# Performance work log

Hardware: AMD Instinct MI355X
Metric: run time of the kernel (lower is better)

Reference implementation:

```python
import jax, jax.numpy as jnp
import numpy as np

B, N, FIN, FOUT, H = 8, 2048, 128, 128, 2


def setup_inputs() -> dict:
    key = jax.random.key(0)
    k_h, k_adj, k_w, k_a = jax.random.split(key, 4)
    h = jax.random.normal(k_h, (B, N, FIN), dtype=jnp.float32)
    adj = jax.random.randint(k_adj, (B, N, N), 0, 2).astype(jnp.int32)
    # self-loops so no softmax row is all -inf
    idx = jnp.arange(N)
    adj = adj.at[:, idx, idx].set(1)
    W = jax.random.normal(k_w, (H, FIN, FOUT), dtype=jnp.float32) * 0.1
    a = jax.random.normal(k_a, (H, 2 * FOUT), dtype=jnp.float32) * 0.1
    return {"h": h, "adj": adj, "W": W, "a": a}


def reference(h, adj, W, a):
    # h: [B,N,FIN], adj: [B,N,N] int, W: [H,FIN,FOUT], a: [H,2*FOUT]
    Fout = W.shape[-1]
    Wh = jnp.einsum('bnf,hfo->bhno', h, W)              # [B,H,N,FOUT]
    # decompose a^T [Wh_i || Wh_j] = a1.Wh_i + a2.Wh_j (exact same math,
    # avoids the [B,N,N,2F] concat the torch code materializes)
    a1, a2 = a[:, :Fout], a[:, Fout:]
    s_i = jnp.einsum('bhno,ho->bhn', Wh, a1)            # score from node i
    s_j = jnp.einsum('bhno,ho->bhn', Wh, a2)            # score from node j
    e = jax.nn.leaky_relu(s_i[:, :, :, None] + s_j[:, :, None, :], 0.2)  # [B,H,N,N]
    e = jnp.where(adj[:, None, :, :] == 0, -jnp.inf, e)
    att = jax.nn.softmax(e, axis=-1)                    # [B,H,N,N]
    out = jnp.einsum('bhnm,bhmo->bhno', att, Wh)        # [B,H,N,FOUT]
    b, hh, n, f = out.shape
    # concat heads along feature dim (head order matches torch cat)
    return out.transpose(0, 2, 1, 3).reshape(b, n, hh * f)
```

## Files before the change

### kernel.cpp

```cpp
#include <hip/hip_runtime.h>
#include <math.h>

constexpr int Bv   = 8;
constexpr int Nv   = 2048;
constexpr int FIN  = 128;
constexpr int FOUT = 128;
constexpr int NH   = 2;
constexpr float LOG2E = 1.44269504088896340736f;

typedef __attribute__((ext_vector_type(8)))  short short8;
typedef __attribute__((ext_vector_type(4)))  float f32x4;
typedef __attribute__((ext_vector_type(16))) float f32x16;
typedef __attribute__((ext_vector_type(4)))  int   i32x4;
typedef unsigned long long u64;

typedef __attribute__((address_space(1))) const void GCV;
typedef __attribute__((address_space(3))) void LV;

static __device__ __forceinline__ unsigned short f2bf(float f) {
    unsigned u = __builtin_bit_cast(unsigned, f);
    u += 0x7fffu + ((u >> 16) & 1u);
    return (unsigned short)(u >> 16);
}
static __device__ __forceinline__ float bf2f(unsigned short s) {
    unsigned u = ((unsigned)s) << 16;
    return __builtin_bit_cast(float, u);
}
static __device__ __forceinline__ float fast_exp2(float x) {
#if __has_builtin(__builtin_amdgcn_exp2f)
    return __builtin_amdgcn_exp2f(x);
#else
    return exp2f(x);
#endif
}
static __device__ __forceinline__ unsigned cvt_pk_bf16(float lo, float hi) {
    unsigned r;
    asm("v_cvt_pk_bf16_f32 %0, %1, %2" : "=v"(r) : "v"(lo), "v"(hi));
    return r;
}

__global__ __launch_bounds__(256) void wa_kernel(const float* __restrict__ W,
                                                 const float* __restrict__ a,
                                                 float* __restrict__ wa,
                                                 unsigned short* __restrict__ wthi,
                                                 unsigned short* __restrict__ wtlo) {
    __shared__ unsigned short shi[FIN * 132];
    __shared__ unsigned short slo[FIN * 132];
    int hh = blockIdx.x;
    int t = threadIdx.x;

    const float* Ws = W + (size_t)hh * FIN * FOUT;
    for (int idx = t; idx < FIN * FOUT; idx += 256) {
        int f = idx >> 7, o = idx & 127;
        float wv = Ws[idx];
        unsigned short uh = f2bf(wv);
        shi[o * 132 + f] = uh;
        slo[o * 132 + f] = f2bf(wv - bf2f(uh));
    }

    int f = t >> 1, half = t & 1;
    const float* Wr = Ws + (size_t)f * FOUT + half * 64;
    const float* ar = a + (size_t)hh * 2 * FOUT + half * 64;
    float s1 = 0.f, s2 = 0.f;
    for (int o = 0; o < 64; o += 4) {
        float4 w4 = *(const float4*)&Wr[o];
        s1 += w4.x * ar[o] + w4.y * ar[o + 1] + w4.z * ar[o + 2] + w4.w * ar[o + 3];
        s2 += w4.x * ar[FOUT + o] + w4.y * ar[FOUT + o + 1] + w4.z * ar[FOUT + o + 2] + w4.w * ar[FOUT + o + 3];
    }
    s1 += __shfl_xor(s1, 1, 64);
    s2 += __shfl_xor(s2, 1, 64);
    if (half == 0) {
        wa[(hh * 2 + 0) * FIN + f] = s1 * LOG2E;
        wa[(hh * 2 + 1) * FIN + f] = s2 * LOG2E;
    }

    __syncthreads();
    unsigned short* dhi = wthi + (size_t)hh * FOUT * FIN;
    unsigned short* dlo = wtlo + (size_t)hh * FOUT * FIN;
    for (int idx = t; idx < FIN * FOUT; idx += 256) {
        int o = idx >> 7, ff = idx & 127;
        dhi[idx] = shi[o * 132 + ff];
        dlo[idx] = slo[o * 132 + ff];
    }
}

__global__ __launch_bounds__(256, 4) void prep2_kernel(
    const float* __restrict__ h, const float* __restrict__ wa,
    const unsigned short* __restrict__ wthi, const unsigned short* __restrict__ wtlo,
    unsigned short* __restrict__ whf, float* __restrict__ si, float* __restrict__ sj) {
    int bid = blockIdx.x;
    int t   = threadIdx.x;

    if (bid < 4096) {
        int row  = bid * 4 + (t >> 6);
        int lane = t & 63;
        float x0 = h[(size_t)row * FIN + lane];
        float x1 = h[(size_t)row * FIN + 64 + lane];
        float s[4];
#pragma unroll
        for (int q = 0; q < 4; ++q) {
            const float* wp = wa + q * FIN;
            s[q] = x0 * wp[lane] + x1 * wp[64 + lane];
        }
#pragma unroll
        for (int m = 32; m >= 1; m >>= 1) {
#pragma unroll
            for (int q = 0; q < 4; ++q) s[q] += __shfl_xor(s[q], m, 64);
        }
        if (lane == 0) {
            int bb = row >> 11, n = row & (Nv - 1);
            si[((size_t)(bb * NH + 0)) * Nv + n] = s[0];
            sj[((size_t)(bb * NH + 0)) * Nv + n] = s[1];
            si[((size_t)(bb * NH + 1)) * Nv + n] = s[2];
            sj[((size_t)(bb * NH + 1)) * Nv + n] = s[3];
        }
    } else {
        int wb2 = bid - 4096;
        int bb  = wb2 & 7;
        int r2  = wb2 >> 3;
        int hh  = r2 & 1;
        int jtb = r2 >> 1;
        int n0  = jtb * 64;

        int w = t >> 6, l = t & 63, lo16 = l & 15, grp = l >> 4;
        int o0 = w * 32;

        const unsigned short* Whi = wthi + (size_t)hh * FOUT * FIN;
        const unsigned short* Wlo = wtlo + (size_t)hh * FOUT * FIN;
        short8 ahi[2][4], alo[2][4];
#pragma unroll
        for (int ot = 0; ot < 2; ++ot)
#pragma unroll
            for (int kt = 0; kt < 4; ++kt) {
                int off = (o0 + ot * 16 + lo16) * FIN + kt * 32 + grp * 8;
                ahi[ot][kt] = *(const short8*)&Whi[off];
                alo[ot][kt] = *(const short8*)&Wlo[off];
            }

        f32x4 acc[2][4];
#pragma unroll
        for (int ot = 0; ot < 2; ++ot)
#pragma unroll
            for (int nt = 0; nt < 4; ++nt) acc[ot][nt] = (f32x4){0.f, 0.f, 0.f, 0.f};

        const float* hb = h + ((size_t)bb * Nv + n0) * FIN;
#pragma unroll
        for (int nt = 0; nt < 4; ++nt) {
#pragma unroll
            for (int kt = 0; kt < 4; ++kt) {
                const float* hp = hb + (size_t)(nt * 16 + lo16) * FIN + kt * 32 + grp * 8;
                float4 x0 = *(const float4*)hp;
                float4 x1 = *(const float4*)(hp + 4);
                float xs[8] = {x0.x, x0.y, x0.z, x0.w, x1.x, x1.y, x1.z, x1.w};
                short8 bhi, blo;
#pragma unroll
                for (int i = 0; i < 8; ++i) {
                    unsigned short uh = f2bf(xs[i]);
                    bhi[i] = (short)uh;
                    blo[i] = (short)f2bf(xs[i] - bf2f(uh));
                }
#pragma unroll
                for (int ot = 0; ot < 2; ++ot) {
                    acc[ot][nt] = __builtin_amdgcn_mfma_f32_16x16x32_bf16(ahi[ot][kt], bhi, acc[ot][nt], 0, 0, 0);
                    acc[ot][nt] = __builtin_amdgcn_mfma_f32_16x16x32_bf16(ahi[ot][kt], blo, acc[ot][nt], 0, 0, 0);
                    acc[ot][nt] = __builtin_amdgcn_mfma_f32_16x16x32_bf16(alo[ot][kt], bhi, acc[ot][nt], 0, 0, 0);
                }
            }
        }
        unsigned short* db = whf + (size_t)(bb * NH + hh) * 262144;
#pragma unroll
        for (int ot = 0; ot < 2; ++ot)
#pragma unroll
            for (int nt = 0; nt < 4; ++nt)
#pragma unroll
                for (int reg = 0; reg < 4; ++reg) {
                    int oc = ot * 16 + grp * 4 + reg;
                    db[(size_t)(((jtb * 4 + nt) * 4 + w) * 64 + (lo16 >> 3) * 32 + oc) * 8 + (lo16 & 7)] =
                        f2bf(acc[ot][nt][reg]);
                }
    }
}

__global__ __launch_bounds__(256, 2) void gat_mega_kernel(
    const int* __restrict__ adj, const unsigned short* __restrict__ whf,
    const float* __restrict__ si, const float* __restrict__ sj,
    float* __restrict__ out) {
    __shared__ int abuf[2][2][2048];
    __shared__ u64 mlds[32][33];

    int bid = blockIdx.x;
    int bb  = bid & 7;
    int rp  = bid >> 3;
    int r0  = rp * 32;

    int t = threadIdx.x, w = t >> 6, l = t & 63;

    {
        int wr = w >> 1;
        int wsg = w & 1;
        const int* base = adj + ((size_t)bb * Nv + r0) * Nv;

        auto issue = [&](int buf, int c) {
            const int* src = base + (size_t)(c * 2 + wr) * Nv + wsg * 1024 + l * 4;
            LV* dst = (LV*)&abuf[buf][wr][wsg * 1024];
#pragma unroll
            for (int k = 0; k < 4; ++k) {
                __builtin_amdgcn_global_load_lds((GCV*)(src + k * 256),
                                                 (LV*)((char*)dst + k * 1024), 16, 0, 0);
            }
        };

        issue(0, 0);
        int buf = 0;
        for (int c = 0; c < 16; ++c) {
            if (c < 15) issue(buf ^ 1, c + 1);
            if (c < 15) { asm volatile("s_waitcnt vmcnt(4)" ::: "memory"); }
            else        { asm volatile("s_waitcnt vmcnt(0)" ::: "memory"); }
            __builtin_amdgcn_sched_barrier(0);
            u64 myval = 0;
#pragma unroll
            for (int j16 = 0; j16 < 16; ++j16) {
                int jt = wsg * 16 + j16;
                int iv = abuf[buf][wr][jt * 64 + l];
                u64 bal = __ballot(iv != 0);
                if (l == j16) myval = bal;
            }
            if (l < 16) mlds[c * 2 + wr][wsg * 16 + l] = myval;
            buf ^= 1;
        }
    }
    __syncthreads();

    int hh = w >> 1, ch = w & 1;
    int lo32 = l & 31, kh = l >> 5;
    int myrow = r0 + lo32;

    float sir = si[(size_t)(bb * NH + hh) * Nv + myrow];
    const float* sjb  = sj + (size_t)(bb * NH + hh) * Nv;
    const unsigned short* wbp = whf + (size_t)(bb * NH + hh) * 262144 + (size_t)l * 8;

    f32x16 acc0, acc1, accL;
#pragma unroll
    for (int i = 0; i < 16; ++i) { acc0[i] = 0.f; acc1[i] = 0.f; accL[i] = 0.f; }

    const int ones_w = 0x3f803f80;
    short8 onesf = __builtin_bit_cast(short8, (i32x4){ones_w, ones_w, ones_w, ones_w});

    for (int jt = 0; jt < 32; ++jt) {
        int jb = jt * 64;
        const unsigned short* fb = wbp + (size_t)(jt * 16 + ch * 2) * 512;
        short8 bf[4][2];
#pragma unroll
        for (int kt = 0; kt < 4; ++kt) {
            bf[kt][0] = *(const short8*)(fb + (kt * 4 + 0) * 512);
            bf[kt][1] = *(const short8*)(fb + (kt * 4 + 1) * 512);
        }
        u64 mcur = mlds[lo32][jt];

        short8 af[4];
#pragma unroll
        for (int kt = 0; kt < 4; ++kt) {
            unsigned mb = (unsigned)(mcur >> (kt * 16 + kh * 8)) & 0xFFu;
            const float* sp = &sjb[jb + kt * 16 + kh * 8];
            float4 s0 = *(const float4*)sp;
            float4 s1 = *(const float4*)(sp + 4);
            float x0 = sir + s0.x, x1 = sir + s0.y, x2 = sir + s0.z, x3 = sir + s0.w;
            float x4 = sir + s1.x, x5 = sir + s1.y, x6 = sir + s1.z, x7 = sir + s1.w;
            x0 = fmaxf(x0, 0.2f * x0); x1 = fmaxf(x1, 0.2f * x1);
            x2 = fmaxf(x2, 0.2f * x2); x3 = fmaxf(x3, 0.2f * x3);
            x4 = fmaxf(x4, 0.2f * x4); x5 = fmaxf(x5, 0.2f * x5);
            x6 = fmaxf(x6, 0.2f * x6); x7 = fmaxf(x7, 0.2f * x7);
            float p0 = fast_exp2(x0), p1 = fast_exp2(x1), p2 = fast_exp2(x2), p3 = fast_exp2(x3);
            float p4 = fast_exp2(x4), p5 = fast_exp2(x5), p6 = fast_exp2(x6), p7 = fast_exp2(x7);
            p0 = (mb & 1u)   ? p0 : 0.f;  p1 = (mb & 2u)   ? p1 : 0.f;
            p2 = (mb & 4u)   ? p2 : 0.f;  p3 = (mb & 8u)   ? p3 : 0.f;
            p4 = (mb & 16u)  ? p4 : 0.f;  p5 = (mb & 32u)  ? p5 : 0.f;
            p6 = (mb & 64u)  ? p6 : 0.f;  p7 = (mb & 128u) ? p7 : 0.f;
            unsigned w0 = cvt_pk_bf16(p0, p1), w1 = cvt_pk_bf16(p2, p3);
            unsigned w2 = cvt_pk_bf16(p4, p5), w3 = cvt_pk_bf16(p6, p7);
            af[kt] = __builtin_bit_cast(short8, (i32x4){(int)w0, (int)w1, (int)w2, (int)w3});
        }
#pragma unroll
        for (int kt = 0; kt < 4; ++kt) {
            acc0 = __builtin_amdgcn_mfma_f32_32x32x16_bf16(af[kt], bf[kt][0], acc0, 0, 0, 0);
            acc1 = __builtin_amdgcn_mfma_f32_32x32x16_bf16(af[kt], bf[kt][1], acc1, 0, 0, 0);
            accL = __builtin_amdgcn_mfma_f32_32x32x16_bf16(af[kt], onesf,    accL, 0, 0, 0);
        }
    }

#pragma unroll
    for (int reg = 0; reg < 16; ++reg) {
        int rowc = (reg & 3) + 8 * (reg >> 2) + 4 * kh;
        float linv = 1.0f / accL[reg];
        float* op = out + ((size_t)(bb * Nv + r0 + rowc)) * (NH * FOUT) + hh * FOUT + ch * 64;
        op[lo32]      = acc0[reg] * linv;
        op[32 + lo32] = acc1[reg] * linv;
    }
}

extern "C" void kernel_launch(void* const* d_in, const int* in_sizes, int n_in,
                              void* d_out, int out_size, void* d_ws, size_t ws_size,
                              hipStream_t stream) {
    const float* h   = (const float*)d_in[0];
    const int*   adj = (const int*)d_in[1];
    const float* W   = (const float*)d_in[2];
    const float* a   = (const float*)d_in[3];
    float*       out = (float*)d_out;

    char* ws = (char*)d_ws;
    unsigned short* whf  = (unsigned short*)ws;
    float* si = (float*)(ws + 8388608);
    float* sj = si + (size_t)Bv * NH * Nv;
    float* wa = sj + (size_t)Bv * NH * Nv;
    unsigned short* wthi = (unsigned short*)(wa + NH * 2 * FIN);
    unsigned short* wtlo = wthi + (size_t)NH * FOUT * FIN;

    wa_kernel   <<<dim3(2),    dim3(256), 0, stream>>>(W, a, wa, wthi, wtlo);
    prep2_kernel<<<dim3(4608), dim3(256), 0, stream>>>(h, wa, wthi, wtlo, whf, si, sj);
    gat_mega_kernel<<<dim3(512), dim3(256), 0, stream>>>(adj, whf, si, sj, out);
}
```

Before: 107.5 us.

## Interleave adjacency mask streaming with attention MFMA loop

The kernel no longer packs the whole 32x2048 adjacency tile into bitmasks before starting compute. Each iteration now loads a 32x128 column chunk through a double-buffered global_load_lds pipeline, ballots it into a per-buffer mask, synchronizes, and runs the softmax-weighted MFMAs for those two 64-column tiles. The goal is to hide the large adjacency read behind the exp/MFMA work and to cut LDS use, which may allow more occupancy. The cost is a __syncthreads every chunk, and it relies on the vmcnt accounting still covering the outstanding loads correctly.

```diff
diff --git a/kernel.cpp b/kernel.cpp
--- a/kernel.cpp
+++ b/kernel.cpp
@@ -185,8 +185,8 @@
     const int* __restrict__ adj, const unsigned short* __restrict__ whf,
     const float* __restrict__ si, const float* __restrict__ sj,
     float* __restrict__ out) {
-    __shared__ int abuf[2][2][2048];
-    __shared__ u64 mlds[32][33];
+    __shared__ int abuf[2][32][128];
+    __shared__ u64 mlds[2][32][2];
 
     int bid = blockIdx.x;
     int bb  = bid & 7;
@@ -194,47 +194,21 @@
     int r0  = rp * 32;
 
     int t = threadIdx.x, w = t >> 6, l = t & 63;
-
-    {
-        int wr = w >> 1;
-        int wsg = w & 1;
-        const int* base = adj + ((size_t)bb * Nv + r0) * Nv;
-
-        auto issue = [&](int buf, int c) {
-            const int* src = base + (size_t)(c * 2 + wr) * Nv + wsg * 1024 + l * 4;
-            LV* dst = (LV*)&abuf[buf][wr][wsg * 1024];
-#pragma unroll
-            for (int k = 0; k < 4; ++k) {
-                __builtin_amdgcn_global_load_lds((GCV*)(src + k * 256),
-                                                 (LV*)((char*)dst + k * 1024), 16, 0, 0);
-            }
-        };
-
-        issue(0, 0);
-        int buf = 0;
-        for (int c = 0; c < 16; ++c) {
-            if (c < 15) issue(buf ^ 1, c + 1);
-            if (c < 15) { asm volatile("s_waitcnt vmcnt(4)" ::: "memory"); }
-            else        { asm volatile("s_waitcnt vmcnt(0)" ::: "memory"); }
-            __builtin_amdgcn_sched_barrier(0);
-            u64 myval = 0;
-#pragma unroll
-            for (int j16 = 0; j16 < 16; ++j16) {
-                int jt = wsg * 16 + j16;
-                int iv = abuf[buf][wr][jt * 64 + l];
-                u64 bal = __ballot(iv != 0);
-                if (l == j16) myval = bal;
-            }
-            if (l < 16) mlds[c * 2 + wr][wsg * 16 + l] = myval;
-            buf ^= 1;
-        }
-    }
-    __syncthreads();
-
     int hh = w >> 1, ch = w & 1;
     int lo32 = l & 31, kh = l >> 5;
     int myrow = r0 + lo32;
 
+    const int* gbase = adj + ((size_t)bb * Nv + r0 + w * 8) * Nv;
+
+    auto issue = [&](int buf, int c) {
+#pragma unroll
+        for (int k = 0; k < 4; ++k) {
+            const int* src = gbase + (size_t)(2 * k + (l >> 5)) * Nv + c * 128 + (l & 31) * 4;
+            LV* dst = (LV*)&abuf[buf][w * 8 + 2 * k][0];
+            __builtin_amdgcn_global_load_lds((GCV*)src, dst, 16, 0, 0);
+        }
+    };
+
     float sir = si[(size_t)(bb * NH + hh) * Nv + myrow];
     const float* sjb  = sj + (size_t)(bb * NH + hh) * Nv;
     const unsigned short* wbp = whf + (size_t)(bb * NH + hh) * 262144 + (size_t)l * 8;
@@ -246,46 +220,71 @@
     const int ones_w = 0x3f803f80;
     short8 onesf = __builtin_bit_cast(short8, (i32x4){ones_w, ones_w, ones_w, ones_w});
 
-    for (int jt = 0; jt < 32; ++jt) {
-        int jb = jt * 64;
-        const unsigned short* fb = wbp + (size_t)(jt * 16 + ch * 2) * 512;
-        short8 bf[4][2];
-#pragma unroll
-        for (int kt = 0; kt < 4; ++kt) {
-            bf[kt][0] = *(const short8*)(fb + (kt * 4 + 0) * 512);
-            bf[kt][1] = *(const short8*)(fb + (kt * 4 + 1) * 512);
-        }
-        u64 mcur = mlds[lo32][jt];
-
-        short8 af[4];
-#pragma unroll
-        for (int kt = 0; kt < 4; ++kt) {
-            unsigned mb = (unsigned)(mcur >> (kt * 16 + kh * 8)) & 0xFFu;
-            const float* sp = &sjb[jb + kt * 16 + kh * 8];
-            float4 s0 = *(const float4*)sp;
-            float4 s1 = *(const float4*)(sp + 4);
-            float x0 = sir + s0.x, x1 = sir + s0.y, x2 = sir + s0.z, x3 = sir + s0.w;
-            float x4 = sir + s1.x, x5 = sir + s1.y, x6 = sir + s1.z, x7 = sir + s1.w;
-            x0 = fmaxf(x0, 0.2f * x0); x1 = fmaxf(x1, 0.2f * x1);
-            x2 = fmaxf(x2, 0.2f * x2); x3 = fmaxf(x3, 0.2f * x3);
-            x4 = fmaxf(x4, 0.2f * x4); x5 = fmaxf(x5, 0.2f * x5);
-            x6 = fmaxf(x6, 0.2f * x6); x7 = fmaxf(x7, 0.2f * x7);
-            float p0 = fast_exp2(x0), p1 = fast_exp2(x1), p2 = fast_exp2(x2), p3 = fast_exp2(x3);
-            float p4 = fast_exp2(x4), p5 = fast_exp2(x5), p6 = fast_exp2(x6), p7 = fast_exp2(x7);
-            p0 = (mb & 1u)   ? p0 : 0.f;  p1 = (mb & 2u)   ? p1 : 0.f;
-            p2 = (mb & 4u)   ? p2 : 0.f;  p3 = (mb & 8u)   ? p3 : 0.f;
-            p4 = (mb & 16u)  ? p4 : 0.f;  p5 = (mb & 32u)  ? p5 : 0.f;
-            p6 = (mb & 64u)  ? p6 : 0.f;  p7 = (mb & 128u) ? p7 : 0.f;
-            unsigned w0 = cvt_pk_bf16(p0, p1), w1 = cvt_pk_bf16(p2, p3);
-            unsigned w2 = cvt_pk_bf16(p4, p5), w3 = cvt_pk_bf16(p6, p7);
-            af[kt] = __builtin_bit_cast(short8, (i32x4){(int)w0, (int)w1, (int)w2, (int)w3});
-        }
-#pragma unroll
-        for (int kt = 0; kt < 4; ++kt) {
-            acc0 = __builtin_amdgcn_mfma_f32_32x32x16_bf16(af[kt], bf[kt][0], acc0, 0, 0, 0);
-            acc1 = __builtin_amdgcn_mfma_f32_32x32x16_bf16(af[kt], bf[kt][1], acc1, 0, 0, 0);
-            accL = __builtin_amdgcn_mfma_f32_32x32x16_bf16(af[kt], onesf,    accL, 0, 0, 0);
-        }
+    issue(0, 0);
+    int buf = 0;
+    for (int c = 0; c < 16; ++c) {
+        if (c < 15) {
+            issue(buf ^ 1, c + 1);
+            asm volatile("s_waitcnt vmcnt(4)" ::: "memory");
+        } else {
+            asm volatile("s_waitcnt vmcnt(0)" ::: "memory");
+        }
+        __builtin_amdgcn_sched_barrier(0);
+#pragma unroll
+        for (int r = 0; r < 8; ++r) {
+            int row = w * 8 + r;
+#pragma unroll
+            for (int q = 0; q < 2; ++q) {
+                int iv = abuf[buf][row][q * 64 + l];
+                u64 bal = __ballot(iv != 0);
+                if (l == 0) mlds[buf][row][q] = bal;
+            }
+        }
+        __syncthreads();
+#pragma unroll
+        for (int q = 0; q < 2; ++q) {
+            int jt = 2 * c + q;
+            int jb = jt * 64;
+            const unsigned short* fb = wbp + (size_t)(jt * 16 + ch * 2) * 512;
+            short8 bf[4][2];
+#pragma unroll
+            for (int kt = 0; kt < 4; ++kt) {
+                bf[kt][0] = *(const short8*)(fb + (kt * 4 + 0) * 512);
+                bf[kt][1] = *(const short8*)(fb + (kt * 4 + 1) * 512);
+            }
+            u64 mcur = mlds[buf][lo32][q];
+
+            short8 af[4];
+#pragma unroll
+            for (int kt = 0; kt < 4; ++kt) {
+                unsigned mb = (unsigned)(mcur >> (kt * 16 + kh * 8)) & 0xFFu;
+                const float* sp = &sjb[jb + kt * 16 + kh * 8];
+                float4 s0 = *(const float4*)sp;
+                float4 s1 = *(const float4*)(sp + 4);
+                float x0 = sir + s0.x, x1 = sir + s0.y, x2 = sir + s0.z, x3 = sir + s0.w;
+                float x4 = sir + s1.x, x5 = sir + s1.y, x6 = sir + s1.z, x7 = sir + s1.w;
+                x0 = fmaxf(x0, 0.2f * x0); x1 = fmaxf(x1, 0.2f * x1);
+                x2 = fmaxf(x2, 0.2f * x2); x3 = fmaxf(x3, 0.2f * x3);
+                x4 = fmaxf(x4, 0.2f * x4); x5 = fmaxf(x5, 0.2f * x5);
+                x6 = fmaxf(x6, 0.2f * x6); x7 = fmaxf(x7, 0.2f * x7);
+                float p0 = fast_exp2(x0), p1 = fast_exp2(x1), p2 = fast_exp2(x2), p3 = fast_exp2(x3);
+                float p4 = fast_exp2(x4), p5 = fast_exp2(x5), p6 = fast_exp2(x6), p7 = fast_exp2(x7);
+                p0 = (mb & 1u)   ? p0 : 0.f;  p1 = (mb & 2u)   ? p1 : 0.f;
+                p2 = (mb & 4u)   ? p2 : 0.f;  p3 = (mb & 8u)   ? p3 : 0.f;
+                p4 = (mb & 16u)  ? p4 : 0.f;  p5 = (mb & 32u)  ? p5 : 0.f;
+                p6 = (mb & 64u)  ? p6 : 0.f;  p7 = (mb & 128u) ? p7 : 0.f;
+                unsigned w0 = cvt_pk_bf16(p0, p1), w1 = cvt_pk_bf16(p2, p3);
+                unsigned w2 = cvt_pk_bf16(p4, p5), w3 = cvt_pk_bf16(p6, p7);
+                af[kt] = __builtin_bit_cast(short8, (i32x4){(int)w0, (int)w1, (int)w2, (int)w3});
+            }
+#pragma unroll
+            for (int kt = 0; kt < 4; ++kt) {
+                acc0 = __builtin_amdgcn_mfma_f32_32x32x16_bf16(af[kt], bf[kt][0], acc0, 0, 0, 0);
+                acc1 = __builtin_amdgcn_mfma_f32_32x32x16_bf16(af[kt], bf[kt][1], acc1, 0, 0, 0);
+                accL = __builtin_amdgcn_mfma_f32_32x32x16_bf16(af[kt], onesf,    accL, 0, 0, 0);
+            }
+        }
+        buf ^= 1;
     }
 
 #pragma unroll
```

After: 115.2 us. +7.1%, slower.
